# Performance work log

Measured on AMD Instinct MI355X. Metric: run time of the kernel, lower is better.

The kernel has to match this reference:

```python
import jax, jax.numpy as jnp
import numpy as np

B, L, D, DF, E, R = 4, 1024, 1024, 4096, 32768, 64
EPS = 1e-6


def layer_norm(x, g, b, eps=EPS):
    mu = x.mean(-1, keepdims=True)
    var = ((x - mu) ** 2).mean(-1, keepdims=True)
    return (x - mu) * jax.lax.rsqrt(var + eps) * g + b


def setup_inputs() -> dict:
    key = jax.random.key(0)
    ks = jax.random.split(key, 16)
    s = 0.02
    return {
        "hidden_states": jax.random.normal(ks[0], (B, L, D), jnp.float32),
        "rel_table": jax.random.normal(ks[1], (R, D), jnp.float32) * s,
        "Wq": jax.random.normal(ks[2], (D, D), jnp.float32) * s,
        "bq": jnp.zeros((D,), jnp.float32),
        "Wk": jax.random.normal(ks[3], (D, D), jnp.float32) * s,
        "Wv": jax.random.normal(ks[4], (D, D), jnp.float32) * s,
        "Wo": jax.random.normal(ks[5], (D, D), jnp.float32) * s,
        "bo": jnp.zeros((D,), jnp.float32),
        "ln0_g": jnp.ones((D,), jnp.float32),
        "ln0_b": jnp.zeros((D,), jnp.float32),
        "ln1_g": jnp.ones((D,), jnp.float32),
        "ln1_b": jnp.zeros((D,), jnp.float32),
        "W1": jax.random.normal(ks[6], (D, DF), jnp.float32) * s,
        "b1": jnp.zeros((DF,), jnp.float32),
        "W2": jax.random.normal(ks[7], (DF, D), jnp.float32) * s,
        "b2": jnp.zeros((D,), jnp.float32),
        "ln2_g": jnp.ones((D,), jnp.float32),
        "ln2_b": jnp.zeros((D,), jnp.float32),
        "edge_src": jax.random.randint(ks[8], (B, E), 0, L, jnp.int32),
        "edge_dst": jax.random.randint(ks[9], (B, E), 0, L, jnp.int32),
        "edge_rel": jax.random.randint(ks[10], (B, E), 0, R, jnp.int32),
    }


def reference(hidden_states, rel_table, Wq, bq, Wk, Wv, Wo, bo,
              ln0_g, ln0_b, ln1_g, ln1_b, W1, b1, W2, b2, ln2_g, ln2_b,
              edge_src, edge_dst, edge_rel):
    scale = np.sqrt(D).astype(np.float32)  # num_heads=1 -> d_k = D
    hs_norm = layer_norm(hidden_states, ln0_g, ln0_b)

    def rgat_one(x, src, dst, rel):
        # x: [L, D]; src/dst/rel: [E]
        e = rel_table[rel]                       # [E, D] relation embeddings
        q = x @ Wq + bq
        k = x @ Wk
        v = x @ Wv
        score = jnp.sum((k[src] + e) * q[dst], axis=-1) / scale      # [E]
        score = jnp.exp(jnp.clip(score, -10.0, 10.0))
        wv = jax.ops.segment_sum((v[src] + e) * score[:, None], dst, num_segments=L)
        z = jax.ops.segment_sum(score, dst, num_segments=L)          # [L]
        o = wv / z[:, None]
        out = layer_norm(x + o @ Wo + bo, ln1_g, ln1_b)
        ffn = jnp.maximum(out @ W1 + b1, 0.0) @ W2 + b2
        return layer_norm(out + ffn, ln2_g, ln2_b)

    graph_rep = jax.vmap(rgat_one)(hs_norm, edge_src, edge_dst, edge_rel)
    out = jax.nn.elu(graph_rep)                  # dropout = identity (eval)
    return hidden_states + out
```

## Files before the change

kernel.cpp:

```cpp
#include <hip/hip_runtime.h>
#include <hip/hip_bf16.h>

#define B_SZ 4
#define L_SEQ 1024
#define D_MODEL 1024
#define DF_FF 4096
#define E_PER_B 32768
#define R_REL 64
#define M_ROWS (B_SZ * L_SEQ)

typedef __attribute__((ext_vector_type(8))) short bf16x8;
typedef __attribute__((ext_vector_type(4))) float f32x4;

__device__ inline float b2f(unsigned short u) {
    union { unsigned int i; float f; } x; x.i = ((unsigned int)u) << 16; return x.f;
}
__device__ inline unsigned short f2b(float f) {
    union { float f; unsigned int u; } x; x.f = f;
    unsigned int r = x.u + 0x7FFFu + ((x.u >> 16) & 1u);
    return (unsigned short)(r >> 16);
}

#define GLOBAL_CAST(p) ((const __attribute__((address_space(1))) void*)(p))
#define LDS_CAST(p)    ((__attribute__((address_space(3))) void*)(p))

#define BT_QKV (1024u * 3072u)
#define SEXT_M 1152
#define LDA_WV 1088
#define LDB_WVP 1152
#define BT_WVP (1024u * 1152u)

__global__ void prep_all(const float* __restrict__ Wq, const float* __restrict__ Wk,
                         const float* __restrict__ Wv, const float* __restrict__ Wo,
                         const float* __restrict__ W1, const float* __restrict__ W2,
                         const float* __restrict__ rel, const float* __restrict__ bq,
                         const float* __restrict__ hidden,
                         const float* __restrict__ ln0_g, const float* __restrict__ ln0_b,
                         unsigned short* __restrict__ Wqkv_t, unsigned short* __restrict__ Wo_t,
                         unsigned short* __restrict__ W1_t, unsigned short* __restrict__ W2_t,
                         unsigned short* __restrict__ relbPad,
                         float* __restrict__ bqkv,
                         unsigned short* __restrict__ Xn_b16,
                         float* __restrict__ zeroReg) {
    __shared__ float tile[32][33];
    __shared__ float sb1[4], sb2[4];
    const int id = blockIdx.x, tid = threadIdx.x;
    if (id < 12288) {
        const float* src; unsigned short* dst; int K, N, x, y;
        if (id < 4096) {
            const int seg = id >> 10, t = id & 1023;
            K = 1024; N = 1024; x = t & 31; y = t >> 5;
            src = (seg == 0) ? Wq : (seg == 1) ? Wk : (seg == 2) ? Wv : Wo;
            dst = (seg == 3) ? Wo_t : (Wqkv_t + (size_t)seg * 1048576);
        } else if (id < 8192) {
            const int t = id - 4096; K = 1024; N = 4096; x = t & 127; y = t >> 7;
            src = W1; dst = W1_t;
        } else {
            const int t = id - 8192; K = 4096; N = 1024; x = t & 31; y = t >> 5;
            src = W2; dst = W2_t;
        }
        const int n0 = x * 32, k0 = y * 32, tx = tid & 31, ty = tid >> 5;
#pragma unroll
        for (int r = 0; r < 32; r += 8)
            tile[ty + r][tx] = src[(size_t)(k0 + ty + r) * N + (n0 + tx)];
        __syncthreads();
#pragma unroll
        for (int r = 0; r < 32; r += 8)
            dst[(size_t)(n0 + ty + r) * K + (k0 + tx)] = f2b(tile[tx][ty + r]);
    } else if (id < 12800) {
        const int i = (id - 12288) * 256 + tid;
        relbPad[i] = (i < 65536) ? f2b(rel[i]) : (unsigned short)0;
    } else if (id < 12812) {
        const int i = (id - 12800) * 256 + tid;
        bqkv[i] = (i < 1024) ? bq[i] : 0.0f;
    } else if (id < 16908) {
        const int row = id - 12812, t = tid;
        const size_t base = (size_t)row * 1024 + t * 4;
        float4 xv = *(const float4*)(hidden + base);
        float x0 = xv.x, x1 = xv.y, x2 = xv.z, x3 = xv.w;
        float s = x0 + x1 + x2 + x3;
#pragma unroll
        for (int o = 32; o > 0; o >>= 1) s += __shfl_down(s, o);
        if ((t & 63) == 0) sb1[t >> 6] = s;
        __syncthreads();
        const float mu = (sb1[0] + sb1[1] + sb1[2] + sb1[3]) * (1.0f / 1024.0f);
        const float d0 = x0 - mu, d1 = x1 - mu, d2 = x2 - mu, d3 = x3 - mu;
        float s2 = d0 * d0 + d1 * d1 + d2 * d2 + d3 * d3;
#pragma unroll
        for (int o = 32; o > 0; o >>= 1) s2 += __shfl_down(s2, o);
        if ((t & 63) == 0) sb2[t >> 6] = s2;
        __syncthreads();
        const float var = (sb2[0] + sb2[1] + sb2[2] + sb2[3]) * (1.0f / 1024.0f);
        const float rstd = rsqrtf(var + 1e-6f);
        const float4 gv = *(const float4*)(ln0_g + t * 4);
        const float4 bv = *(const float4*)(ln0_b + t * 4);
        ushort4 ob;
        ob.x = f2b(d0 * rstd * gv.x + bv.x);
        ob.y = f2b(d1 * rstd * gv.y + bv.y);
        ob.z = f2b(d2 * rstd * gv.z + bv.z);
        ob.w = f2b(d3 * rstd * gv.w + bv.w);
        *(ushort4*)(Xn_b16 + base) = ob;
    } else {
        const size_t base = (size_t)(id - 16908) * 4096 + tid * 4;
        const float4 z4 = make_float4(0.f, 0.f, 0.f, 0.f);
#pragma unroll
        for (int j = 0; j < 4; j++)
            *(float4*)(zeroReg + base + j * 1024) = z4;
    }
}

__device__ inline void tile_swizzle(int id, int ntn, int& tm, int& tn) {
    tm = ((id & 7) + ((id >> 3) / ntn) * 8) * 128;
    tn = ((id >> 3) % ntn) * 128;
}

__device__ inline void tile_swizzle2(int id, int ntn, int& tm, int& tn) {
    const int xcd = id & 7;
    const int local = id >> 3;
    const int nh = ntn >> 2;
    tm = ((xcd >> 2) * 16 + (local & 15)) * 128;
    tn = ((xcd & 3) * nh + (local >> 4)) * 128;
}

#define GEMM_BODY(GA, LDA_, GB, LDB_, KLEN)                                                 \
    f32x4 acc[4][4];                                                                        \
    _Pragma("unroll") for (int i = 0; i < 4; i++)                                           \
        _Pragma("unroll") for (int j = 0; j < 4; j++) acc[i][j] = (f32x4)0.0f;              \
    for (int k0 = 0; k0 < (KLEN); k0 += 64) {                                               \
        __syncthreads();                                                                    \
        _Pragma("unroll") for (int r = 0; r < 4; ++r) {                                     \
            __builtin_amdgcn_global_load_lds(GLOBAL_CAST((GA) + (size_t)r * 8 * (LDA_)),    \
                LDS_CAST(&lA[(wave * 32 + r * 8) * 64]), 16, 0, 0);                         \
            __builtin_amdgcn_global_load_lds(GLOBAL_CAST((GB) + (size_t)r * 8 * (LDB_)),    \
                LDS_CAST(&lB[(wave * 32 + r * 8) * 64]), 16, 0, 0);                         \
        }                                                                                   \
        (GA) += 64; (GB) += 64;                                                             \
        __builtin_amdgcn_s_waitcnt(0);                                                      \
        __syncthreads();                                                                    \
        _Pragma("unroll") for (int kk = 0; kk < 2; ++kk) {                                  \
            const int cb = kk * 4 + quad;                                                   \
            bf16x8 af[4], bf[4];                                                            \
            _Pragma("unroll") for (int i = 0; i < 4; i++) {                                 \
                const int ra = wm + i * 16 + l16;                                           \
                af[i] = *(const bf16x8*)&lA[ra * 64 + ((cb ^ (ra & 7)) * 8)];               \
                const int rb = wn + i * 16 + l16;                                           \
                bf[i] = *(const bf16x8*)&lB[rb * 64 + ((cb ^ (rb & 7)) * 8)];               \
            }                                                                               \
            _Pragma("unroll") for (int mi = 0; mi < 4; mi++)                                \
                _Pragma("unroll") for (int ni = 0; ni < 4; ni++)                            \
                    acc[mi][ni] = __builtin_amdgcn_mfma_f32_16x16x32_bf16(                  \
                        af[mi], bf[ni], acc[mi][ni], 0, 0, 0);                              \
        }                                                                                   \
    }

template<bool OUT_BF16, bool RELU, bool SW2>
__global__ __launch_bounds__(256, 4)
void gemm_bf16(const unsigned short* __restrict__ A, int lda,
               const unsigned short* __restrict__ Bt, int ldb, size_t bt_batch,
               const float* __restrict__ bias,
               float* __restrict__ Cf, unsigned short* __restrict__ Cb,
               int N, int K, int ntn) {
    __shared__ unsigned short lA[128 * 64];
    __shared__ unsigned short lB[128 * 64];
    int tile_m, tile_n;
    if (SW2) tile_swizzle2(blockIdx.x, ntn, tile_m, tile_n);
    else     tile_swizzle(blockIdx.x, ntn, tile_m, tile_n);
    const int t = threadIdx.x;
    const int wave = t >> 6, lane = t & 63;
    const int wm = (wave >> 1) * 64, wn = (wave & 1) * 64;
    const int quad = lane >> 4, l16 = lane & 15;
    const int srow = lane >> 3;
    const int schunk = ((lane & 7) ^ srow) * 8;
    const unsigned short* gA = A + (size_t)(tile_m + wave * 32 + srow) * lda + schunk;
    const unsigned short* gB = Bt + (size_t)(tile_m >> 10) * bt_batch
                                  + (size_t)(tile_n + wave * 32 + srow) * ldb + schunk;
    GEMM_BODY(gA, lda, gB, ldb, K)
#pragma unroll
    for (int mi = 0; mi < 4; mi++) {
#pragma unroll
        for (int ni = 0; ni < 4; ni++) {
            const int col = tile_n + wn + ni * 16 + l16;
            const float bv = bias[col];
#pragma unroll
            for (int r = 0; r < 4; r++) {
                const int row = tile_m + wm + mi * 16 + quad * 4 + r;
                float v = acc[mi][ni][r] + bv;
                if (RELU) v = fmaxf(v, 0.0f);
                if (OUT_BF16) Cb[(size_t)row * N + col] = f2b(v);
                else          Cf[(size_t)row * N + col] = v;
            }
        }
    }
}

__global__ __launch_bounds__(256, 4)
void gemm_bf16_splitk(const unsigned short* __restrict__ A, int lda,
                      const unsigned short* __restrict__ Bt, int ldb, size_t bt_batch,
                      const float* __restrict__ bias,
                      unsigned short* __restrict__ Pbase, size_t pstride,
                      int N, int Kc, int ntn) {
    __shared__ unsigned short lA[128 * 64];
    __shared__ unsigned short lB[128 * 64];
    int tile_m, tile_n;
    tile_swizzle(blockIdx.x, ntn, tile_m, tile_n);
    const int z = blockIdx.z;
    const int kofs = z * Kc;
    const int t = threadIdx.x;
    const int wave = t >> 6, lane = t & 63;
    const int wm = (wave >> 1) * 64, wn = (wave & 1) * 64;
    const int quad = lane >> 4, l16 = lane & 15;
    const int srow = lane >> 3;
    const int schunk = ((lane & 7) ^ srow) * 8;
    const unsigned short* gA = A + (size_t)(tile_m + wave * 32 + srow) * lda + kofs + schunk;
    const unsigned short* gB = Bt + (size_t)(tile_m >> 10) * bt_batch
                                  + (size_t)(tile_n + wave * 32 + srow) * ldb + kofs + schunk;
    GEMM_BODY(gA, lda, gB, ldb, Kc)
    unsigned short* P = Pbase + (size_t)z * pstride;
#pragma unroll
    for (int mi = 0; mi < 4; mi++) {
#pragma unroll
        for (int ni = 0; ni < 4; ni++) {
            const int col = tile_n + wn + ni * 16 + l16;
            const float bv = (z == 0) ? bias[col] : 0.0f;
#pragma unroll
            for (int r = 0; r < 4; r++) {
                const int row = tile_m + wm + mi * 16 + quad * 4 + r;
                P[(size_t)row * N + col] = f2b(acc[mi][ni][r] + bv);
            }
        }
    }
}

__global__ __launch_bounds__(256, 4)
void sext_w(const unsigned short* __restrict__ QKV,
            const unsigned short* __restrict__ relPad,
            const unsigned short* __restrict__ Wo_t,
            unsigned short* __restrict__ Pbase,
            unsigned short* __restrict__ Bwvp, int Kc) {
    __shared__ unsigned short lA[128 * 64];
    __shared__ unsigned short lB[128 * 64];
    const int id = blockIdx.x, t = threadIdx.x;
    const int wave = t >> 6, lane = t & 63;
    const int wm = (wave >> 1) * 64, wn = (wave & 1) * 64;
    const int quad = lane >> 4, l16 = lane & 15;
    const int srow = lane >> 3;
    const int schunk = ((lane & 7) ^ srow) * 8;

    if (id >= 576) {
        const int t2 = id - 576;
        const int b = t2 / 72, rem = t2 % 72;
        const int tile_m = (rem / 9) * 128;
        const int tile_n = (rem % 9) * 128;
        const unsigned short* gA = Wo_t + (size_t)(tile_m + wave * 32 + srow) * 1024 + schunk;
        const int brow = tile_n + wave * 32 + srow;
        const unsigned short* gB;
        size_t ldb;
        if (tile_n < 1024) {
            gB = QKV + (size_t)b * BT_QKV + (size_t)brow * 3072 + 2048 + schunk;
            ldb = 3072;
        } else {
            gB = relPad + (size_t)(brow - 1024) * 1024 + schunk;
            ldb = 1024;
        }
        GEMM_BODY(gA, 1024, gB, ldb, 1024)
        unsigned short* P = Bwvp + (size_t)b * BT_WVP;
#pragma unroll
        for (int mi = 0; mi < 4; mi++) {
#pragma unroll
            for (int ni = 0; ni < 4; ni++) {
                const int col = tile_n + wn + ni * 16 + l16;
#pragma unroll
                for (int r = 0; r < 4; r++) {
                    const int row = tile_m + wm + mi * 16 + quad * 4 + r;
                    P[(size_t)row * LDB_WVP + col] = f2b(acc[mi][ni][r]);
                }
            }
        }
        return;
    }

    const int bx = id % 72, b = (id / 72) & 3, z = id / 288;
    const int tile_m = (bx >> 3) * 128;
    const int tile_n = (bx & 7) * 128;
    const int kofs = z * Kc;
    const int arow = tile_m + wave * 32 + srow;
    const unsigned short* gA;
    size_t lda;
    if (tile_m < 1024) {
        gA = QKV + (size_t)b * BT_QKV + (size_t)arow * 3072 + 1024 + kofs + schunk;
        lda = 3072;
    } else {
        gA = relPad + (size_t)(arow - 1024) * 1024 + kofs + schunk;
        lda = 1024;
    }
    const unsigned short* gB = QKV + (size_t)b * BT_QKV
                                   + (size_t)(tile_n + wave * 32 + srow) * 3072 + kofs + schunk;
    GEMM_BODY(gA, lda, gB, 3072, Kc)
    unsigned short* P = Pbase + ((size_t)z * B_SZ + b) * (SEXT_M * 1024);
#pragma unroll
    for (int mi = 0; mi < 4; mi++) {
#pragma unroll
        for (int ni = 0; ni < 4; ni++) {
            const int col = tile_n + wn + ni * 16 + l16;
#pragma unroll
            for (int r = 0; r < 4; r++) {
                const int row = tile_m + wm + mi * 16 + quad * 4 + r;
                P[(size_t)row * 1024 + col] = f2b(acc[mi][ni][r]);
            }
        }
    }
}

__global__ __launch_bounds__(256, 4)
void gemm_wv_splitk(const unsigned short* __restrict__ A,
                    const unsigned short* __restrict__ Bt,
                    const float* __restrict__ bias,
                    unsigned short* __restrict__ Pbase, size_t pstride) {
    __shared__ unsigned short lA[128 * 64];
    __shared__ unsigned short lB[128 * 64];
    int tile_m, tile_n;
    tile_swizzle(blockIdx.x, 8, tile_m, tile_n);
    const int z = blockIdx.z;
    const int kofs = z * 576;
    const int Kc = z ? 512 : 576;
    const int t = threadIdx.x;
    const int wave = t >> 6, lane = t & 63;
    const int wm = (wave >> 1) * 64, wn = (wave & 1) * 64;
    const int quad = lane >> 4, l16 = lane & 15;
    const int srow = lane >> 3;
    const int schunk = ((lane & 7) ^ srow) * 8;
    const unsigned short* gA = A + (size_t)(tile_m + wave * 32 + srow) * LDA_WV + kofs + schunk;
    const unsigned short* gB = Bt + (size_t)(tile_m >> 10) * BT_WVP
                                  + (size_t)(tile_n + wave * 32 + srow) * LDB_WVP + kofs + schunk;
    GEMM_BODY(gA, LDA_WV, gB, LDB_WVP, Kc)
    unsigned short* P = Pbase + (size_t)z * pstride;
#pragma unroll
    for (int mi = 0; mi < 4; mi++) {
#pragma unroll
        for (int ni = 0; ni < 4; ni++) {
            const int col = tile_n + wn + ni * 16 + l16;
            const float bv = (z == 0) ? bias[col] : 0.0f;
#pragma unroll
            for (int r = 0; r < 4; r++) {
                const int row = tile_m + wm + mi * 16 + quad * 4 + r;
                P[(size_t)row * 1024 + col] = f2b(acc[mi][ni][r] + bv);
            }
        }
    }
}

template<bool FINAL, int NR>
__global__ void ln_kernel(const unsigned short* __restrict__ Xb,
                          const unsigned short* __restrict__ Rbase, size_t rstride,
                          const float* __restrict__ g, const float* __restrict__ be,
                          unsigned short* __restrict__ ob16,
                          const float* __restrict__ hidden, float* __restrict__ fout) {
    __shared__ float sb1[4], sb2[4];
    const int row = blockIdx.x, t = threadIdx.x;
    const size_t base = (size_t)row * 1024 + t * 4;

    ushort4 xv = *(const ushort4*)(Xb + base);
    float x0 = b2f(xv.x), x1 = b2f(xv.y), x2 = b2f(xv.z), x3 = b2f(xv.w);
#pragma unroll
    for (int r = 0; r < NR; r++) {
        ushort4 rv = *(const ushort4*)(Rbase + r * rstride + base);
        x0 += b2f(rv.x); x1 += b2f(rv.y); x2 += b2f(rv.z); x3 += b2f(rv.w);
    }
    float s = x0 + x1 + x2 + x3;
#pragma unroll
    for (int o = 32; o > 0; o >>= 1) s += __shfl_down(s, o);
    if ((t & 63) == 0) sb1[t >> 6] = s;
    __syncthreads();
    const float mu = (sb1[0] + sb1[1] + sb1[2] + sb1[3]) * (1.0f / 1024.0f);

    const float d0 = x0 - mu, d1 = x1 - mu, d2 = x2 - mu, d3 = x3 - mu;
    float s2 = d0 * d0 + d1 * d1 + d2 * d2 + d3 * d3;
#pragma unroll
    for (int o = 32; o > 0; o >>= 1) s2 += __shfl_down(s2, o);
    if ((t & 63) == 0) sb2[t >> 6] = s2;
    __syncthreads();
    const float var = (sb2[0] + sb2[1] + sb2[2] + sb2[3]) * (1.0f / 1024.0f);
    const float rstd = rsqrtf(var + 1e-6f);

    const float4 gv = *(const float4*)(g + t * 4);
    const float4 bv = *(const float4*)(be + t * 4);
    const float y0 = d0 * rstd * gv.x + bv.x;
    const float y1 = d1 * rstd * gv.y + bv.y;
    const float y2 = d2 * rstd * gv.z + bv.z;
    const float y3 = d3 * rstd * gv.w + bv.w;

    if (!FINAL) {
        ushort4 ob; ob.x = f2b(y0); ob.y = f2b(y1); ob.z = f2b(y2); ob.w = f2b(y3);
        *(ushort4*)(ob16 + base) = ob;
    } else {
        const float4 hv = *(const float4*)(hidden + base);
        const float e0 = y0 > 0.0f ? y0 : expm1f(y0);
        const float e1 = y1 > 0.0f ? y1 : expm1f(y1);
        const float e2 = y2 > 0.0f ? y2 : expm1f(y2);
        const float e3 = y3 > 0.0f ? y3 : expm1f(y3);
        float4 o; o.x = hv.x + e0; o.y = hv.y + e1; o.z = hv.z + e2; o.w = hv.w + e3;
        *(float4*)(fout + base) = o;
    }
}

__global__ void edge_scatter(const unsigned short* __restrict__ S,
                             const int* __restrict__ src, const int* __restrict__ dst,
                             const int* __restrict__ rel,
                             float* __restrict__ A, float* __restrict__ G) {
    const size_t ZSTR = (size_t)B_SZ * SEXT_M * 1024;
    const int gg = blockIdx.x * 256 + threadIdx.x;
    const int b = gg >> 15;
    const int s = src[gg], d = dst[gg], r = rel[gg];
    const size_t sbase = ((size_t)b * SEXT_M + s) * 1024 + d;
    const size_t tbase = ((size_t)b * SEXT_M + 1024 + r) * 1024 + d;
    const float sval = b2f(S[sbase]) + b2f(S[sbase + ZSTR]);
    const float tval = b2f(S[tbase]) + b2f(S[tbase + ZSTR]);
    float sc = (sval + tval) * (1.0f / 32.0f);
    sc = expf(fminf(fmaxf(sc, -10.0f), 10.0f));
    atomicAdd(&A[((size_t)((b << 10) + d) << 10) + s], sc);
    atomicAdd(&G[((size_t)((b << 10) + d) << 6) + r], sc);
}

__global__ void normalize(const float* __restrict__ A, const float* __restrict__ G,
                          unsigned short* __restrict__ Awv) {
    __shared__ float sInv;
    const int row = blockIdx.x, t = threadIdx.x;
    float v = 0.0f;
    if (t < 64) {
        v = G[(size_t)row * 64 + t];
        float s = v;
#pragma unroll
        for (int o = 1; o < 64; o <<= 1) s += __shfl_xor(s, o);
        if (t == 0) sInv = 1.0f / s;
    }
    __syncthreads();
    const float inv = sInv;
    const size_t obase = (size_t)row * LDA_WV;
    const float4 a = *(const float4*)(A + (size_t)row * 1024 + t * 4);
    ushort4 o;
    o.x = f2b(a.x * inv); o.y = f2b(a.y * inv); o.z = f2b(a.z * inv); o.w = f2b(a.w * inv);
    *(ushort4*)(Awv + obase + t * 4) = o;
    if (t < 16) {
        const float4 gq = *(const float4*)(G + (size_t)row * 64 + t * 4);
        ushort4 og;
        og.x = f2b(gq.x * inv); og.y = f2b(gq.y * inv);
        og.z = f2b(gq.z * inv); og.w = f2b(gq.w * inv);
        *(ushort4*)(Awv + obase + 1024 + t * 4) = og;
    }
}

extern "C" void kernel_launch(void* const* d_in, const int* in_sizes, int n_in,
                              void* d_out, int out_size, void* d_ws, size_t ws_size,
                              hipStream_t stream) {
    const float* hidden  = (const float*)d_in[0];
    const float* rel_tbl = (const float*)d_in[1];
    const float* Wq = (const float*)d_in[2];
    const float* bq = (const float*)d_in[3];
    const float* Wk = (const float*)d_in[4];
    const float* Wv = (const float*)d_in[5];
    const float* Wo = (const float*)d_in[6];
    const float* bo = (const float*)d_in[7];
    const float* ln0_g = (const float*)d_in[8];
    const float* ln0_b = (const float*)d_in[9];
    const float* ln1_g = (const float*)d_in[10];
    const float* ln1_b = (const float*)d_in[11];
    const float* W1 = (const float*)d_in[12];
    const float* b1 = (const float*)d_in[13];
    const float* W2 = (const float*)d_in[14];
    const float* b2 = (const float*)d_in[15];
    const float* ln2_g = (const float*)d_in[16];
    const float* ln2_b = (const float*)d_in[17];
    const int* esrc = (const int*)d_in[18];
    const int* edst = (const int*)d_in[19];
    const int* erel = (const int*)d_in[20];
    float* out = (float*)d_out;

    char* ws = (char*)d_ws;
    const size_t MB = 1024 * 1024;
    unsigned short* Xn_b16  = (unsigned short*)(ws + 16 * MB);
    unsigned short* H1      = (unsigned short*)(ws + 0);
    unsigned short* Wqkv_t  = (unsigned short*)(ws + 24 * MB);
    unsigned short* Wo_t    = (unsigned short*)(ws + 30 * MB);
    unsigned short* W1_t    = (unsigned short*)(ws + 32 * MB);
    unsigned short* W2_t    = (unsigned short*)(ws + 40 * MB);
    unsigned short* relbPad = (unsigned short*)(ws + 48 * MB);
    float*          bqkv    = (float*)(ws + 48 * MB + 512 * 1024);
    unsigned short* QKV     = (unsigned short*)(ws + 49 * MB);
    unsigned short* Awv     = (unsigned short*)(ws + 49 * MB);
    unsigned short* Qw2H    = (unsigned short*)(ws + 49 * MB);
    unsigned short* PwoH    = (unsigned short*)(ws + 66 * MB);
    unsigned short* SxH     = (unsigned short*)(ws + 73 * MB);
    unsigned short* Bwvp    = (unsigned short*)(ws + 92 * MB);
    float*          Amat    = (float*)(ws + 101 * MB);
    float*          Gmat    = (float*)(ws + 117 * MB);
    unsigned short* Out_b16 = (unsigned short*)(ws + 113 * MB);

    const size_t PSTRIDE_H = 4u * 1024 * 1024;
    const dim3 blk(256);

    prep_all<<<17996, blk, 0, stream>>>(Wq, Wk, Wv, Wo, W1, W2, rel_tbl, bq,
                                        hidden, ln0_g, ln0_b,
                                        Wqkv_t, Wo_t, W1_t, W2_t, relbPad, bqkv,
                                        Xn_b16, Amat);
    gemm_bf16<true, false, true><<<dim3(24 * 32), blk, 0, stream>>>(
        Xn_b16, 1024, Wqkv_t, 1024, 0, bqkv, nullptr, QKV, 3072, 1024, 24);
    sext_w<<<864, blk, 0, stream>>>(QKV, relbPad, Wo_t, SxH, Bwvp, 512);
    edge_scatter<<<512, blk, 0, stream>>>(SxH, esrc, edst, erel, Amat, Gmat);
    normalize<<<M_ROWS, blk, 0, stream>>>(Amat, Gmat, Awv);
    gemm_wv_splitk<<<dim3(256, 1, 2), blk, 0, stream>>>(Awv, Bwvp, bo, PwoH, PSTRIDE_H);
    ln_kernel<false, 2><<<M_ROWS, blk, 0, stream>>>(Xn_b16, PwoH, PSTRIDE_H, ln1_g, ln1_b,
                                                    Out_b16, nullptr, nullptr);
    gemm_bf16<true, true, true><<<dim3(32 * 32), blk, 0, stream>>>(
        Out_b16, 1024, W1_t, 1024, 0, b1, nullptr, H1, 4096, 1024, 32);
    gemm_bf16_splitk<<<dim3(8 * 32, 1, 4), blk, 0, stream>>>(
        H1, 4096, W2_t, 4096, 0, b2, Qw2H, PSTRIDE_H, 1024, 1024, 8);
    ln_kernel<true, 4><<<M_ROWS, blk, 0, stream>>>(Out_b16, Qw2H, PSTRIDE_H, ln2_g, ln2_b,
                                                   nullptr, hidden, out);
    (void)in_sizes; (void)n_in; (void)out_size; (void)ws_size;
}
```

Measured before the change: 354.3 us.

## Replace 128x128 GEMMs with 256x256 double-buffered 8-wave pipelined GEMM kernel

```diff
diff --git a/kernel.cpp b/kernel.cpp
--- a/kernel.cpp
+++ b/kernel.cpp
@@ -113,13 +113,9 @@
     tm = ((id & 7) + ((id >> 3) / ntn) * 8) * 128;
     tn = ((id >> 3) % ntn) * 128;
 }
-
-__device__ inline void tile_swizzle2(int id, int ntn, int& tm, int& tn) {
-    const int xcd = id & 7;
-    const int local = id >> 3;
-    const int nh = ntn >> 2;
-    tm = ((xcd >> 2) * 16 + (local & 15)) * 128;
-    tn = ((xcd & 3) * nh + (local >> 4)) * 128;
+__device__ inline void tsw256(int id, int ntn, int& tm, int& tn) {
+    tm = ((id & 7) + ((id >> 3) / ntn) * 8) * 256;
+    tn = ((id >> 3) % ntn) * 256;
 }
 
 #define GEMM_BODY(GA, LDA_, GB, LDB_, KLEN)                                                 \
@@ -153,79 +149,125 @@
         }                                                                                   \
     }
 
-template<bool OUT_BF16, bool RELU, bool SW2>
-__global__ __launch_bounds__(256, 4)
-void gemm_bf16(const unsigned short* __restrict__ A, int lda,
-               const unsigned short* __restrict__ Bt, int ldb, size_t bt_batch,
-               const float* __restrict__ bias,
-               float* __restrict__ Cf, unsigned short* __restrict__ Cb,
-               int N, int K, int ntn) {
-    __shared__ unsigned short lA[128 * 64];
-    __shared__ unsigned short lB[128 * 64];
+#define ST_A(bufc, hh, kt) { \
+    __builtin_amdgcn_global_load_lds(GLOBAL_CAST(gA[hh][0] + (kt) * 64), \
+        LDS_CAST(&ls[bufc][0][((hh) * 128 + wv * 8) * 64]), 16, 0, 0); \
+    __builtin_amdgcn_global_load_lds(GLOBAL_CAST(gA[hh][1] + (kt) * 64), \
+        LDS_CAST(&ls[bufc][0][((hh) * 128 + 64 + wv * 8) * 64]), 16, 0, 0); }
+#define ST_B(bufc, hh, kt) { \
+    __builtin_amdgcn_global_load_lds(GLOBAL_CAST(gB[hh][0] + (kt) * 64), \
+        LDS_CAST(&ls[bufc][1][((hh) * 128 + wv * 8) * 64]), 16, 0, 0); \
+    __builtin_amdgcn_global_load_lds(GLOBAL_CAST(gB[hh][1] + (kt) * 64), \
+        LDS_CAST(&ls[bufc][1][((hh) * 128 + 64 + wv * 8) * 64]), 16, 0, 0); }
+
+#define PHASE(bufc, hh, gg, STMT, WAITSTMT) { \
+    bf16x8 paf[4][2], pbf[2][2]; \
+    _Pragma("unroll") for (int m4 = 0; m4 < 4; m4++) { \
+        const int ra = ((hh) * 128 + wm * 64 + m4 * 16 + l16) * 64; \
+        _Pragma("unroll") for (int kk = 0; kk < 2; kk++) \
+            paf[m4][kk] = *(const bf16x8*)&ls[bufc][0][ra + (((kk * 4 + quad) ^ (l16 & 7)) * 8)]; \
+    } \
+    _Pragma("unroll") for (int ng = 0; ng < 2; ng++) { \
+        const int rb2 = ((gg) * 128 + wc * 32 + ng * 16 + l16) * 64; \
+        _Pragma("unroll") for (int kk = 0; kk < 2; kk++) \
+            pbf[ng][kk] = *(const bf16x8*)&ls[bufc][1][rb2 + (((kk * 4 + quad) ^ (l16 & 7)) * 8)]; \
+    } \
+    STMT; \
+    asm volatile("s_waitcnt lgkmcnt(8)"); \
+    __builtin_amdgcn_s_barrier(); \
+    asm volatile("s_waitcnt lgkmcnt(0)"); \
+    __builtin_amdgcn_sched_barrier(0); \
+    __builtin_amdgcn_s_setprio(1); \
+    _Pragma("unroll") for (int m4 = 0; m4 < 4; m4++) \
+        _Pragma("unroll") for (int ng = 0; ng < 2; ng++) \
+            _Pragma("unroll") for (int kk = 0; kk < 2; kk++) \
+                acc[(hh) * 4 + m4][(gg) * 2 + ng] = __builtin_amdgcn_mfma_f32_16x16x32_bf16( \
+                    paf[m4][kk], pbf[ng][kk], acc[(hh) * 4 + m4][(gg) * 2 + ng], 0, 0, 0); \
+    __builtin_amdgcn_s_setprio(0); \
+    WAITSTMT; \
+    __builtin_amdgcn_s_barrier(); }
+
+template<bool RELU, bool SPLITK>
+__global__ __launch_bounds__(512, 2)
+void gemm256(const unsigned short* __restrict__ A, int lda,
+             const unsigned short* __restrict__ Bt, int ldb,
+             const float* __restrict__ bias,
+             unsigned short* __restrict__ C, size_t pstride,
+             int N, int Kc, int ntn) {
+    __shared__ unsigned short ls[2][2][16384];
     int tile_m, tile_n;
-    if (SW2) tile_swizzle2(blockIdx.x, ntn, tile_m, tile_n);
-    else     tile_swizzle(blockIdx.x, ntn, tile_m, tile_n);
+    tsw256(blockIdx.x, ntn, tile_m, tile_n);
     const int t = threadIdx.x;
-    const int wave = t >> 6, lane = t & 63;
-    const int wm = (wave >> 1) * 64, wn = (wave & 1) * 64;
+    const int wv = t >> 6, lane = t & 63;
+    const int wm = wv >> 2;
+    const int wc = wv & 3;
     const int quad = lane >> 4, l16 = lane & 15;
-    const int srow = lane >> 3;
-    const int schunk = ((lane & 7) ^ srow) * 8;
-    const unsigned short* gA = A + (size_t)(tile_m + wave * 32 + srow) * lda + schunk;
-    const unsigned short* gB = Bt + (size_t)(tile_m >> 10) * bt_batch
-                                  + (size_t)(tile_n + wave * 32 + srow) * ldb + schunk;
-    GEMM_BODY(gA, lda, gB, ldb, K)
-#pragma unroll
-    for (int mi = 0; mi < 4; mi++) {
+    const int srow8 = lane >> 3;
+    const int schunk = ((lane & 7) ^ srow8) * 8;
+    const int z = SPLITK ? blockIdx.z : 0;
+    const int kofs = z * Kc;
+
+    const unsigned short* gA[2][2];
+    const unsigned short* gB[2][2];
+#pragma unroll
+    for (int h = 0; h < 2; h++)
+#pragma unroll
+        for (int j = 0; j < 2; j++) {
+            const int rb = h * 2 + j;
+            const int lb = ((rb & 1) << 1) | (rb >> 1);
+            gA[h][j] = A + (size_t)(tile_m + lb * 64 + wv * 8 + srow8) * lda + kofs + schunk;
+            const int nb = (j * 2 + (wv >> 2)) * 64 + h * 32 + (wv & 3) * 8;
+            gB[h][j] = Bt + (size_t)(tile_n + nb + srow8) * ldb + kofs + schunk;
+        }
+
+    f32x4 acc[8][4];
+#pragma unroll
+    for (int i = 0; i < 8; i++)
+#pragma unroll
+        for (int j = 0; j < 4; j++) acc[i][j] = (f32x4)0.0f;
+
+    ST_A(0, 0, 0); ST_B(0, 0, 0); ST_A(0, 1, 0); ST_B(0, 1, 0);
+    ST_A(1, 0, 1); ST_B(1, 0, 1);
+    asm volatile("s_waitcnt vmcnt(4)");
+    __builtin_amdgcn_s_barrier();
+
+    const int NI = Kc >> 7;
+    for (int it = 0; it < NI - 1; ++it) {
+        const int s1 = 2 * it + 1, s2 = 2 * it + 2, s3 = 2 * it + 3;
+        PHASE(0, 0, 0, ST_A(1, 1, s1), );
+        PHASE(0, 0, 1, ST_B(1, 1, s1), );
+        PHASE(0, 1, 0, ST_A(0, 0, s2), );
+        PHASE(0, 1, 1, ST_B(0, 0, s2), asm volatile("s_waitcnt vmcnt(4)"));
+        PHASE(1, 0, 0, ST_A(0, 1, s2), );
+        PHASE(1, 0, 1, ST_B(0, 1, s2), );
+        PHASE(1, 1, 0, ST_A(1, 0, s3), );
+        PHASE(1, 1, 1, ST_B(1, 0, s3), asm volatile("s_waitcnt vmcnt(4)"));
+    }
+    {
+        const int sl = 2 * NI - 1;
+        PHASE(0, 0, 0, ST_A(1, 1, sl), );
+        PHASE(0, 0, 1, ST_B(1, 1, sl), );
+        PHASE(0, 1, 0, , );
+        PHASE(0, 1, 1, , asm volatile("s_waitcnt vmcnt(0)"));
+        PHASE(1, 0, 0, , );
+        PHASE(1, 0, 1, , );
+        PHASE(1, 1, 0, , );
+        PHASE(1, 1, 1, , );
+    }
+
+    unsigned short* Co = C + (SPLITK ? (size_t)z * pstride : 0);
+#pragma unroll
+    for (int mi = 0; mi < 8; mi++) {
 #pragma unroll
         for (int ni = 0; ni < 4; ni++) {
-            const int col = tile_n + wn + ni * 16 + l16;
-            const float bv = bias[col];
+            const int col = tile_n + wc * 64 + ni * 16 + l16;
+            const float bv = (SPLITK && z != 0) ? 0.0f : bias[col];
 #pragma unroll
             for (int r = 0; r < 4; r++) {
-                const int row = tile_m + wm + mi * 16 + quad * 4 + r;
+                const int row = tile_m + wm * 128 + mi * 16 + quad * 4 + r;
                 float v = acc[mi][ni][r] + bv;
                 if (RELU) v = fmaxf(v, 0.0f);
-                if (OUT_BF16) Cb[(size_t)row * N + col] = f2b(v);
-                else          Cf[(size_t)row * N + col] = v;
-            }
-        }
-    }
-}
-
-__global__ __launch_bounds__(256, 4)
-void gemm_bf16_splitk(const unsigned short* __restrict__ A, int lda,
-                      const unsigned short* __restrict__ Bt, int ldb, size_t bt_batch,
-                      const float* __restrict__ bias,
-                      unsigned short* __restrict__ Pbase, size_t pstride,
-                      int N, int Kc, int ntn) {
-    __shared__ unsigned short lA[128 * 64];
-    __shared__ unsigned short lB[128 * 64];
-    int tile_m, tile_n;
-    tile_swizzle(blockIdx.x, ntn, tile_m, tile_n);
-    const int z = blockIdx.z;
-    const int kofs = z * Kc;
-    const int t = threadIdx.x;
-    const int wave = t >> 6, lane = t & 63;
-    const int wm = (wave >> 1) * 64, wn = (wave & 1) * 64;
-    const int quad = lane >> 4, l16 = lane & 15;
-    const int srow = lane >> 3;
-    const int schunk = ((lane & 7) ^ srow) * 8;
-    const unsigned short* gA = A + (size_t)(tile_m + wave * 32 + srow) * lda + kofs + schunk;
-    const unsigned short* gB = Bt + (size_t)(tile_m >> 10) * bt_batch
-                                  + (size_t)(tile_n + wave * 32 + srow) * ldb + kofs + schunk;
-    GEMM_BODY(gA, lda, gB, ldb, Kc)
-    unsigned short* P = Pbase + (size_t)z * pstride;
-#pragma unroll
-    for (int mi = 0; mi < 4; mi++) {
-#pragma unroll
-        for (int ni = 0; ni < 4; ni++) {
-            const int col = tile_n + wn + ni * 16 + l16;
-            const float bv = (z == 0) ? bias[col] : 0.0f;
-#pragma unroll
-            for (int r = 0; r < 4; r++) {
-                const int row = tile_m + wm + mi * 16 + quad * 4 + r;
-                P[(size_t)row * N + col] = f2b(acc[mi][ni][r] + bv);
+                Co[(size_t)row * N + col] = f2b(v);
             }
         }
     }
@@ -497,23 +539,24 @@
 
     const size_t PSTRIDE_H = 4u * 1024 * 1024;
     const dim3 blk(256);
+    const dim3 blk512(512);
 
     prep_all<<<17996, blk, 0, stream>>>(Wq, Wk, Wv, Wo, W1, W2, rel_tbl, bq,
                                         hidden, ln0_g, ln0_b,
                                         Wqkv_t, Wo_t, W1_t, W2_t, relbPad, bqkv,
                                         Xn_b16, Amat);
-    gemm_bf16<true, false, true><<<dim3(24 * 32), blk, 0, stream>>>(
-        Xn_b16, 1024, Wqkv_t, 1024, 0, bqkv, nullptr, QKV, 3072, 1024, 24);
+    gemm256<false, false><<<dim3(192), blk512, 0, stream>>>(
+        Xn_b16, 1024, Wqkv_t, 1024, bqkv, QKV, 0, 3072, 1024, 12);
     sext_w<<<864, blk, 0, stream>>>(QKV, relbPad, Wo_t, SxH, Bwvp, 512);
     edge_scatter<<<512, blk, 0, stream>>>(SxH, esrc, edst, erel, Amat, Gmat);
     normalize<<<M_ROWS, blk, 0, stream>>>(Amat, Gmat, Awv);
     gemm_wv_splitk<<<dim3(256, 1, 2), blk, 0, stream>>>(Awv, Bwvp, bo, PwoH, PSTRIDE_H);
     ln_kernel<false, 2><<<M_ROWS, blk, 0, stream>>>(Xn_b16, PwoH, PSTRIDE_H, ln1_g, ln1_b,
                                                     Out_b16, nullptr, nullptr);
-    gemm_bf16<true, true, true><<<dim3(32 * 32), blk, 0, stream>>>(
-        Out_b16, 1024, W1_t, 1024, 0, b1, nullptr, H1, 4096, 1024, 32);
-    gemm_bf16_splitk<<<dim3(8 * 32, 1, 4), blk, 0, stream>>>(
-        H1, 4096, W2_t, 4096, 0, b2, Qw2H, PSTRIDE_H, 1024, 1024, 8);
+    gemm256<true, false><<<dim3(256), blk512, 0, stream>>>(
+        Out_b16, 1024, W1_t, 1024, b1, H1, 0, 4096, 1024, 16);
+    gemm256<false, true><<<dim3(64, 1, 4), blk512, 0, stream>>>(
+        H1, 4096, W2_t, 4096, b2, Qw2H, PSTRIDE_H, 1024, 1024, 4);
     ln_kernel<true, 4><<<M_ROWS, blk, 0, stream>>>(Out_b16, Qw2H, PSTRIDE_H, ln2_g, ln2_b,
                                                    nullptr, hidden, out);
     (void)in_sizes; (void)n_in; (void)out_size; (void)ws_size;
```

Measured after the change: 360.2 us. About the same (+1.6%).
